# Optimization experiments

Hardware: AMD Instinct MI355X
Metric: run time of the kernel (lower is better)

Reference implementation:

```python
import jax, jax.numpy as jnp
import numpy as np

LN_EPS = 1e-5      # torch nn.LayerNorm default
NORM_EPS = 1e-12   # torch F.normalize default


def _layer_norm(x, gamma, beta):
    mu = jnp.mean(x, axis=-1, keepdims=True)
    var = jnp.mean((x - mu) ** 2, axis=-1, keepdims=True)
    return (x - mu) * jax.lax.rsqrt(var + LN_EPS) * gamma + beta


def _l2_normalize_rows(w):
    n = jnp.sqrt(jnp.sum(w * w, axis=1, keepdims=True))
    return w / jnp.maximum(n, NORM_EPS)


def setup_inputs() -> dict:
    key = jax.random.key(0)
    B, D = 32768, 512
    ks = jax.random.split(key, 4)
    return {
        "stimulus": jax.random.normal(ks[0], (B, D), dtype=jnp.float32),
        "prev_activation": jax.random.normal(ks[1], (B, D), dtype=jnp.float32),
        "W": jax.random.normal(ks[2], (D, D), dtype=jnp.float32),
        "Wr": jax.random.normal(ks[3], (D, D), dtype=jnp.float32),
        "alpha": jnp.full((D,), 0.1, dtype=jnp.float32),
        "decay": jnp.full((D,), 0.01, dtype=jnp.float32),
        "ln_act_gamma": jnp.ones((D,), dtype=jnp.float32),
        "ln_act_beta": jnp.zeros((D,), dtype=jnp.float32),
        "ln_rec_gamma": jnp.ones((D,), dtype=jnp.float32),
        "ln_rec_beta": jnp.zeros((D,), dtype=jnp.float32),
    }


def reference(stimulus, prev_activation, W, Wr, alpha, decay,
              ln_act_gamma, ln_act_beta, ln_rec_gamma, ln_rec_beta):
    # recurrent path
    rec_out = prev_activation @ Wr                      # [B, D]
    rec_norm = _layer_norm(rec_out, ln_rec_gamma, ln_rec_beta)
    # stimulus path
    stim_out = stimulus @ W                             # [B, D]
    final = jax.nn.relu(stim_out + rec_norm)
    final = _layer_norm(final, ln_act_gamma, ln_act_beta)

    # Hebbian weight update (detached in the original module)
    heb_upd = jnp.einsum('bi,bj->ij', stimulus, stim_out) * alpha[None, :]
    rec_upd = jnp.einsum('bi,bj->ij', prev_activation, rec_out) * alpha[None, :]
    # diag(decay) @ W is a row-wise broadcast scale
    new_W = _l2_normalize_rows(W + heb_upd - decay[:, None] * W)
    new_Wr = _l2_normalize_rows(Wr + rec_upd - decay[:, None] * Wr)

    return final, new_W, new_Wr
```

## Files before the change

### kernel.cpp

```cpp
#include <hip/hip_runtime.h>
#include <stdint.h>

typedef unsigned int u32;
typedef unsigned short u16;
typedef float  f32x4 __attribute__((ext_vector_type(4)));
typedef u32    u32x4 __attribute__((ext_vector_type(4)));
typedef __bf16 bf16x8 __attribute__((ext_vector_type(8)));

static __device__ __forceinline__ u16 f2bf(float f){
  u32 u = __builtin_bit_cast(u32, f);
  return (u16)((u + 0x7FFFu + ((u >> 16) & 1u)) >> 16);
}

static __device__ __forceinline__ void async16(const void* g, void* l){
  __builtin_amdgcn_global_load_lds((const __attribute__((address_space(1))) u32*)g,
                                   (__attribute__((address_space(3))) u32*)l, 16, 0, 0);
}

static __device__ __forceinline__ float wave_sum(float v){
#pragma unroll
  for (int o = 32; o > 0; o >>= 1) v += __shfl_xor(v, o, 64);
  return v;
}

__global__ __launch_bounds__(256) void k_cvt(const float* __restrict__ s0, const float* __restrict__ s1,
                                             u16* __restrict__ d0, u16* __restrict__ d1){
  const float* __restrict__ src = blockIdx.y ? s1 : s0;
  u16* __restrict__ dst = blockIdx.y ? d1 : d0;
  size_t i = ((size_t)blockIdx.x*256 + threadIdx.x) * 8;
  f32x4 a = *(const f32x4*)(src + i);
  f32x4 b = *(const f32x4*)(src + i + 4);
  u32x4 w;
  w[0] = (u32)f2bf(a[0]) | ((u32)f2bf(a[1]) << 16);
  w[1] = (u32)f2bf(a[2]) | ((u32)f2bf(a[3]) << 16);
  w[2] = (u32)f2bf(b[0]) | ((u32)f2bf(b[1]) << 16);
  w[3] = (u32)f2bf(b[2]) | ((u32)f2bf(b[3]) << 16);
  *(u32x4*)(dst + i) = w;
}

__global__ __launch_bounds__(256) void k_tp(const u16* __restrict__ s0, const u16* __restrict__ s1,
                                            u16* __restrict__ d0, u16* __restrict__ d1){
  const u16* __restrict__ src = blockIdx.z ? s1 : s0;
  u16* __restrict__ dst = blockIdx.z ? d1 : d0;
  __shared__ u32 st[64*128];
  const int r0 = blockIdx.x * 256;
  const int c0 = blockIdx.y * 64;
  const int t = threadIdx.x;
  const int tb = t & 127, th = t >> 7;
  const u16* pA = src + (size_t)(r0 + 2*tb)*512 + c0 + th*32;
  u32 a[16], b[16];
  {
    u32x4 a0 = *(const u32x4*)pA,        a1 = *(const u32x4*)(pA + 8);
    u32x4 a2 = *(const u32x4*)(pA + 16), a3 = *(const u32x4*)(pA + 24);
    u32x4 b0 = *(const u32x4*)(pA + 512),  b1 = *(const u32x4*)(pA + 520);
    u32x4 b2 = *(const u32x4*)(pA + 528),  b3 = *(const u32x4*)(pA + 536);
#pragma unroll
    for (int e = 0; e < 4; ++e){
      a[e] = a0[e]; a[4+e] = a1[e]; a[8+e] = a2[e]; a[12+e] = a3[e];
      b[e] = b0[e]; b[4+e] = b1[e]; b[8+e] = b2[e]; b[12+e] = b3[e];
    }
  }
  const int g5 = tb >> 2, w2 = tb & 3;
#pragma unroll
  for (int m = 0; m < 16; ++m){
    u32 lo = a[m], hi = b[m];
    u32 w0 = (lo & 0xFFFFu) | (hi << 16);
    u32 w1 = (lo >> 16) | (hi & 0xFFFF0000u);
    int d0i = th*32 + 2*m, d1i = d0i + 1;
    st[d0i*128 + ((g5 ^ (d0i & 7)) << 2) + w2] = w0;
    st[d1i*128 + ((g5 ^ (d1i & 7)) << 2) + w2] = w1;
  }
  __syncthreads();
  const int rd = t >> 2, rg = t & 3;
  u16* drow = dst + (size_t)(c0 + rd)*32768 + r0;
#pragma unroll
  for (int k = 0; k < 8; ++k){
    int gp = rg + 4*k;
    int slot = gp ^ (rd & 7);
    u32x4 w = *(const u32x4*)(st + rd*128 + slot*4);
    *(u32x4*)(drow + rg*8 + 32*k) = w;
  }
}

__global__ __launch_bounds__(256) void k_tcvt(const float* __restrict__ s0, const float* __restrict__ s1,
                                              u16* __restrict__ d0, u16* __restrict__ d1,
                                              int R, int C){
  const float* __restrict__ src = blockIdx.z ? s1 : s0;
  u16* __restrict__ dst = blockIdx.z ? d1 : d0;
  __shared__ u16 lt[64*72];
  const int c0 = blockIdx.x * 64, r0 = blockIdx.y * 64;
  const int tid = threadIdx.x;
  const int rr = tid >> 4, c4 = tid & 15;
#pragma unroll
  for (int p = 0; p < 4; ++p){
    int r = rr + p*16;
    f32x4 f = *(const f32x4*)(src + (size_t)(r0 + r)*C + c0 + c4*4);
#pragma unroll
    for (int e = 0; e < 4; ++e) lt[(c4*4 + e)*72 + r] = f2bf(f[e]);
  }
  __syncthreads();
  const int c = tid >> 2, bg = tid & 3;
  const u32x4* lp = (const u32x4*)(lt + c*72 + bg*16);
  u32x4 w0 = lp[0], w1 = lp[1];
  u16* drow = dst + (size_t)(c0 + c)*R + r0 + bg*16;
  *(u32x4*)drow = w0;
  *(u32x4*)(drow + 8) = w1;
}

__global__ __launch_bounds__(512) void k_gemm_fwd(const u16* __restrict__ SN, const u16* __restrict__ PN,
                                                  const u16* __restrict__ Wt, const u16* __restrict__ Wrt,
                                                  u16* __restrict__ SO, u16* __restrict__ RO,
                                                  u16* __restrict__ SOT, u16* __restrict__ ROT){
  __shared__ char smem[67584];
  u16* sA = (u16*)smem;
  u16* sB = (u16*)(smem + 32768);
  const int tid = threadIdx.x;
  const int lane = tid & 63, wid = tid >> 6;
  const int wm = wid >> 1, wn = wid & 1;
  const int l15 = lane & 15, q = lane >> 4;
  const int id = blockIdx.x;
  const int c8 = id & 7, g = id >> 3;
  const int sel = g >> 6, h = g & 63;
  const int yb = c8*16 + (h >> 2), xb = h & 3;
  const int m0 = yb * 256, n0 = xb * 128;
  const u16* __restrict__ A  = sel ? PN  : SN;
  const u16* __restrict__ Bt = sel ? Wrt : Wt;
  u16* __restrict__ Cn = sel ? RO  : SO;
  u16* __restrict__ Ct = sel ? ROT : SOT;

  f32x4 acc[4][4];
  const f32x4 vzero = {0.f, 0.f, 0.f, 0.f};
#pragma unroll
  for (int a = 0; a < 4; ++a)
#pragma unroll
    for (int b = 0; b < 4; ++b) acc[a][b] = vzero;

#pragma unroll 1
  for (int kt = 0; kt < 8; ++kt){
    const int k0 = kt*64;
#pragma unroll
    for (int it = 0; it < 4; ++it){
      int gg0 = it*512 + tid;
      int r = gg0 >> 3, gp = gg0 & 7, gsw = gp ^ (r & 7);
      async16(A + (size_t)(m0 + r)*512 + k0 + gsw*8, (char*)sA + (size_t)gg0*16);
    }
#pragma unroll
    for (int it = 0; it < 2; ++it){
      int gg0 = it*512 + tid;
      int r = gg0 >> 3, gp = gg0 & 7, gsw = gp ^ (r & 7);
      async16(Bt + (size_t)(n0 + r)*512 + k0 + gsw*8, (char*)sB + (size_t)gg0*16);
    }
    __syncthreads();
#pragma unroll
    for (int kk = 0; kk < 2; ++kk){
      bf16x8 af[4], bfv[4];
#pragma unroll
      for (int mt = 0; mt < 4; ++mt){
        int r = wm*64 + mt*16 + l15;
        int gsw = (kk*4 + q) ^ (r & 7);
        af[mt] = *(const bf16x8*)(sA + (size_t)(r*8 + gsw)*8);
      }
#pragma unroll
      for (int nt = 0; nt < 4; ++nt){
        int r = wn*64 + nt*16 + l15;
        int gsw = (kk*4 + q) ^ (r & 7);
        bfv[nt] = *(const bf16x8*)(sB + (size_t)(r*8 + gsw)*8);
      }
#pragma unroll
      for (int mt = 0; mt < 4; ++mt)
#pragma unroll
        for (int nt = 0; nt < 4; ++nt)
          acc[mt][nt] = __builtin_amdgcn_mfma_f32_16x16x32_bf16(af[mt], bfv[nt], acc[mt][nt], 0, 0, 0);
    }
    __syncthreads();
  }

  u16* lt = (u16*)smem;
#pragma unroll
  for (int mt = 0; mt < 4; ++mt)
#pragma unroll
    for (int nt = 0; nt < 4; ++nt){
      f32x4 v = acc[mt][nt];
      u16 b0 = f2bf(v[0]), b1 = f2bf(v[1]), b2 = f2bf(v[2]), b3 = f2bf(v[3]);
      int n = wn*64 + nt*16 + l15;
      int mb = wm*64 + mt*16 + q*4;
      u16* cn = Cn + (size_t)(m0 + mb)*512 + n0 + n;
      cn[0] = b0; cn[512] = b1; cn[1024] = b2; cn[1536] = b3;
      *(u32*)(lt + n*264 + mb)     = (u32)b0 | ((u32)b1 << 16);
      *(u32*)(lt + n*264 + mb + 2) = (u32)b2 | ((u32)b3 << 16);
    }
  __syncthreads();
#pragma unroll
  for (int p = 0; p < 8; ++p){
    int gg0 = p*512 + tid;
    int n = gg0 >> 5, mg = gg0 & 31;
    u32x4 w = *(const u32x4*)(lt + n*264 + mg*8);
    *(u32x4*)(Ct + (size_t)(n0 + n)*32768 + m0 + mg*8) = w;
  }
}

__global__ __launch_bounds__(512) void k_gemm_upd(const u16* __restrict__ A0, const u16* __restrict__ B0,
                                                  const u16* __restrict__ A1, const u16* __restrict__ B1,
                                                  float* __restrict__ part){
  __shared__ char smem[49152];
  u16* sA = (u16*)smem;
  u16* sB = (u16*)(smem + 16384);
  const int tid = threadIdx.x;
  const int lane = tid & 63, wid = tid >> 6;
  const int wm = wid >> 2, wn = wid & 3;
  const int l15 = lane & 15, q = lane >> 4;
  const int id = blockIdx.x;
  const int c8 = id & 7, g = id >> 3;
  const int zz = c8*8 + (g >> 3);
  const int xy = g & 7;
  const int mat = zz >> 5, sp = zz & 31;
  const int yb = xy & 3, xb = xy >> 2;
  const u16* __restrict__ A = mat ? A1 : A0;
  const u16* __restrict__ B = mat ? B1 : B0;
  const int m0 = yb * 128, n0 = xb * 256;
  const int kb = sp * 1024;

  f32x4 acc[4][4];
  const f32x4 vzero = {0.f, 0.f, 0.f, 0.f};
#pragma unroll
  for (int a = 0; a < 4; ++a)
#pragma unroll
    for (int b = 0; b < 4; ++b) acc[a][b] = vzero;

#pragma unroll 1
  for (int kt = 0; kt < 16; ++kt){
    const int k0 = kb + kt*64;
#pragma unroll
    for (int it = 0; it < 2; ++it){
      int gg0 = it*512 + tid;
      int r = gg0 >> 3, gp = gg0 & 7, gsw = gp ^ (r & 7);
      async16(A + (size_t)(m0 + r)*32768 + k0 + gsw*8, (char*)sA + (size_t)gg0*16);
    }
#pragma unroll
    for (int it = 0; it < 4; ++it){
      int gg0 = it*512 + tid;
      int r = gg0 >> 3, gp = gg0 & 7, gsw = gp ^ (r & 7);
      async16(B + (size_t)(n0 + r)*32768 + k0 + gsw*8, (char*)sB + (size_t)gg0*16);
    }
    __syncthreads();
#pragma unroll
    for (int kk = 0; kk < 2; ++kk){
      bf16x8 af[4], bfv[4];
#pragma unroll
      for (int mt = 0; mt < 4; ++mt){
        int r = wm*64 + mt*16 + l15;
        int gsw = (kk*4 + q) ^ (r & 7);
        af[mt] = *(const bf16x8*)(sA + (size_t)(r*8 + gsw)*8);
      }
#pragma unroll
      for (int nt = 0; nt < 4; ++nt){
        int r = wn*64 + nt*16 + l15;
        int gsw = (kk*4 + q) ^ (r & 7);
        bfv[nt] = *(const bf16x8*)(sB + (size_t)(r*8 + gsw)*8);
      }
#pragma unroll
      for (int mt = 0; mt < 4; ++mt)
#pragma unroll
        for (int nt = 0; nt < 4; ++nt)
          acc[mt][nt] = __builtin_amdgcn_mfma_f32_16x16x32_bf16(af[mt], bfv[nt], acc[mt][nt], 0, 0, 0);
    }
    __syncthreads();
  }

  float* dst = part + (size_t)(mat*32 + sp)*262144;
#pragma unroll
  for (int mt = 0; mt < 4; ++mt)
#pragma unroll
    for (int nt = 0; nt < 4; ++nt){
      f32x4 v = acc[mt][nt];
      int n = wn*64 + nt*16 + l15;
      int mb = wm*64 + mt*16 + q*4;
      float* d = dst + (size_t)(m0 + mb)*512 + n0 + n;
      d[0] = v[0]; d[512] = v[1]; d[1024] = v[2]; d[1536] = v[3];
    }
}

__global__ __launch_bounds__(256) void k_ln(const u16* __restrict__ SO, const u16* __restrict__ RO,
                                            const float* __restrict__ ga, const float* __restrict__ ba,
                                            const float* __restrict__ gr, const float* __restrict__ br,
                                            float* __restrict__ out){
  const int wid = threadIdx.x >> 6, lane = threadIdx.x & 63;
  const size_t b = (size_t)blockIdx.x*4 + wid;
  const int c = lane*8;
  float x[8], t[8];
  {
    u32x4 u = *(const u32x4*)(RO + b*512 + c);
#pragma unroll
    for (int i = 0; i < 4; ++i){
      u32 w = u[i];
      x[2*i]   = __uint_as_float(w << 16);
      x[2*i+1] = __uint_as_float(w & 0xFFFF0000u);
    }
  }
  float s = 0.f, ss = 0.f;
#pragma unroll
  for (int e = 0; e < 8; ++e){ s += x[e]; ss += x[e]*x[e]; }
  s = wave_sum(s); ss = wave_sum(ss);
  float mu = s*(1.f/512.f);
  float var = fmaxf(ss*(1.f/512.f) - mu*mu, 0.f);
  float rs = rsqrtf(var + 1e-5f);
  f32x4 g0 = *(const f32x4*)(gr + c), g1 = *(const f32x4*)(gr + c + 4);
  f32x4 h0 = *(const f32x4*)(br + c), h1 = *(const f32x4*)(br + c + 4);
  {
    u32x4 u = *(const u32x4*)(SO + b*512 + c);
    float so[8];
#pragma unroll
    for (int i = 0; i < 4; ++i){
      u32 w = u[i];
      so[2*i]   = __uint_as_float(w << 16);
      so[2*i+1] = __uint_as_float(w & 0xFFFF0000u);
    }
#pragma unroll
    for (int e = 0; e < 4; ++e) t[e]   = fmaxf(so[e]   + (x[e]  -mu)*rs*g0[e] + h0[e], 0.f);
#pragma unroll
    for (int e = 0; e < 4; ++e) t[4+e] = fmaxf(so[4+e] + (x[4+e]-mu)*rs*g1[e] + h1[e], 0.f);
  }
  float s2 = 0.f, ss2 = 0.f;
#pragma unroll
  for (int e = 0; e < 8; ++e){ s2 += t[e]; ss2 += t[e]*t[e]; }
  s2 = wave_sum(s2); ss2 = wave_sum(ss2);
  float mu2 = s2*(1.f/512.f);
  float var2 = fmaxf(ss2*(1.f/512.f) - mu2*mu2, 0.f);
  float rs2 = rsqrtf(var2 + 1e-5f);
  f32x4 G0 = *(const f32x4*)(ga + c), G1 = *(const f32x4*)(ga + c + 4);
  f32x4 H0 = *(const f32x4*)(ba + c), H1 = *(const f32x4*)(ba + c + 4);
  f32x4 o0, o1;
#pragma unroll
  for (int e = 0; e < 4; ++e){
    o0[e] = (t[e]   - mu2)*rs2*G0[e] + H0[e];
    o1[e] = (t[4+e] - mu2)*rs2*G1[e] + H1[e];
  }
  *(f32x4*)(out + b*512 + c)     = o0;
  *(f32x4*)(out + b*512 + c + 4) = o1;
}

__global__ __launch_bounds__(256) void k_finalize(const float* __restrict__ W0, const float* __restrict__ W1,
                                                  const float* __restrict__ part,
                                                  const float* __restrict__ alpha, const float* __restrict__ decay,
                                                  float* __restrict__ out){
  const int i = blockIdx.x, mat = blockIdx.y;
  const int t = threadIdx.x;
  const float* Wm = mat ? W1 : W0;
  const float* pb = part + (size_t)mat*32*262144 + (size_t)i*512;
  const float dc = decay[i];
  float v[2], ssq = 0.f;
#pragma unroll
  for (int h = 0; h < 2; ++h){
    int j = t + h*256;
    float acc = 0.f;
#pragma unroll
    for (int sp = 0; sp < 32; ++sp) acc += pb[(size_t)sp*262144 + j];
    float val = Wm[(size_t)i*512 + j]*(1.f - dc) + alpha[j]*acc;
    v[h] = val; ssq += val*val;
  }
  float wsum = wave_sum(ssq);
  __shared__ float red[4];
  const int lane = t & 63, wid = t >> 6;
  if (lane == 0) red[wid] = wsum;
  __syncthreads();
  float tot = red[0] + red[1] + red[2] + red[3];
  float rn = 1.f / fmaxf(sqrtf(tot), 1e-12f);
  out[(size_t)mat*262144 + (size_t)i*512 + t]       = v[0]*rn;
  out[(size_t)mat*262144 + (size_t)i*512 + t + 256] = v[1]*rn;
}

extern "C" void kernel_launch(void* const* d_in, const int* in_sizes, int n_in,
                              void* d_out, int out_size, void* d_ws, size_t ws_size,
                              hipStream_t stream) {
  const float* S  = (const float*)d_in[0];
  const float* P  = (const float*)d_in[1];
  const float* W  = (const float*)d_in[2];
  const float* Wr = (const float*)d_in[3];
  const float* alpha = (const float*)d_in[4];
  const float* decay = (const float*)d_in[5];
  const float* ga = (const float*)d_in[6];
  const float* ba = (const float*)d_in[7];
  const float* gr = (const float*)d_in[8];
  const float* br = (const float*)d_in[9];
  float* out = (float*)d_out;

  char* ws = (char*)d_ws;
  const size_t M32 = 33554432;
  const bool big = ws_size >= (size_t)269484032;

  u16 *SN, *PN, *ST, *PT, *SOT, *ROT, *SO, *RO, *Wt, *Wrt;
  if (big){
    SN  = (u16*)(ws);
    PN  = (u16*)(ws + 1*M32);
    ST  = (u16*)(ws + 2*M32);
    PT  = (u16*)(ws + 3*M32);
    SOT = (u16*)(ws + 4*M32);
    ROT = (u16*)(ws + 5*M32);
    SO  = (u16*)(ws + 6*M32);
    RO  = (u16*)(ws + 7*M32);
    Wt  = (u16*)(ws + 8*M32);
    Wrt = (u16*)(ws + 8*M32 + 524288);
  } else {
    SN  = (u16*)(ws);
    PN  = (u16*)(ws + 1*M32);
    SOT = (u16*)(ws + 2*M32);
    ROT = (u16*)(ws + 3*M32);
    SO  = (u16*)(ws + 4*M32);
    RO  = (u16*)(ws + 5*M32);
    Wt  = (u16*)(ws + 6*M32);
    Wrt = (u16*)(ws + 6*M32 + 524288);
    ST  = SO;
    PT  = RO;
  }
  float* part = (float*)ws;

  k_cvt<<<dim3(8192, 2), dim3(256), 0, stream>>>(S, P, SN, PN);
  if (big)
    k_tp<<<dim3(128, 8, 2), dim3(256), 0, stream>>>(SN, PN, ST, PT);
  k_tcvt<<<dim3(8, 8, 2), dim3(256), 0, stream>>>(W, Wr, Wt, Wrt, 512, 512);
  k_gemm_fwd<<<dim3(1024), dim3(512), 0, stream>>>(SN, PN, Wt, Wrt, SO, RO, SOT, ROT);
  k_ln<<<dim3(8192), dim3(256), 0, stream>>>(SO, RO, ga, ba, gr, br, out);
  if (!big)
    k_tp<<<dim3(128, 8, 2), dim3(256), 0, stream>>>(SN, PN, ST, PT);
  k_gemm_upd<<<dim3(512), dim3(512), 0, stream>>>(ST, SOT, PT, ROT, part);
  k_finalize<<<dim3(512, 2), dim3(256), 0, stream>>>(W, Wr, part, alpha, decay, out + 16777216);
}
```

Measured before the change: 346.1 us.

## Fuse input conversion, transpose and weight transpose into one prep kernel

Replaces the separate k_cvt, k_tp and k_tcvt launches with a single k_prep kernel whose blocks are split by index into row-major bf16 conversion, transposed conversion read straight from fp32, and weight transpose-conversion. The transposed copies are now built from the fp32 inputs rather than from the bf16 intermediate, which removes a dependency and two launches. In exchange the fp32 inputs are read twice, and the single shared-memory allocation may lower occupancy for the conversion blocks.

```diff
diff --git a/kernel.cpp b/kernel.cpp
--- a/kernel.cpp
+++ b/kernel.cpp
@@ -23,19 +23,123 @@
   return v;
 }
 
-__global__ __launch_bounds__(256) void k_cvt(const float* __restrict__ s0, const float* __restrict__ s1,
-                                             u16* __restrict__ d0, u16* __restrict__ d1){
-  const float* __restrict__ src = blockIdx.y ? s1 : s0;
-  u16* __restrict__ dst = blockIdx.y ? d1 : d0;
-  size_t i = ((size_t)blockIdx.x*256 + threadIdx.x) * 8;
-  f32x4 a = *(const f32x4*)(src + i);
-  f32x4 b = *(const f32x4*)(src + i + 4);
-  u32x4 w;
-  w[0] = (u32)f2bf(a[0]) | ((u32)f2bf(a[1]) << 16);
-  w[1] = (u32)f2bf(a[2]) | ((u32)f2bf(a[3]) << 16);
-  w[2] = (u32)f2bf(b[0]) | ((u32)f2bf(b[1]) << 16);
-  w[3] = (u32)f2bf(b[2]) | ((u32)f2bf(b[3]) << 16);
-  *(u32x4*)(dst + i) = w;
+
+static __device__ __forceinline__ void prep_cvt(int sub, const float* __restrict__ S,
+                                                const float* __restrict__ P,
+                                                u16* __restrict__ SN, u16* __restrict__ PN){
+  const size_t o0 = ((size_t)sub*256 + threadIdx.x) * 8;
+#pragma unroll
+  for (int j = 0; j < 4; ++j){
+    size_t o = o0 + (size_t)j*4194304;
+    f32x4 a = *(const f32x4*)(S + o);
+    f32x4 b = *(const f32x4*)(S + o + 4);
+    u32x4 w;
+    w[0] = (u32)f2bf(a[0]) | ((u32)f2bf(a[1]) << 16);
+    w[1] = (u32)f2bf(a[2]) | ((u32)f2bf(a[3]) << 16);
+    w[2] = (u32)f2bf(b[0]) | ((u32)f2bf(b[1]) << 16);
+    w[3] = (u32)f2bf(b[2]) | ((u32)f2bf(b[3]) << 16);
+    *(u32x4*)(SN + o) = w;
+  }
+#pragma unroll
+  for (int j = 0; j < 4; ++j){
+    size_t o = o0 + (size_t)j*4194304;
+    f32x4 a = *(const f32x4*)(P + o);
+    f32x4 b = *(const f32x4*)(P + o + 4);
+    u32x4 w;
+    w[0] = (u32)f2bf(a[0]) | ((u32)f2bf(a[1]) << 16);
+    w[1] = (u32)f2bf(a[2]) | ((u32)f2bf(a[3]) << 16);
+    w[2] = (u32)f2bf(b[0]) | ((u32)f2bf(b[1]) << 16);
+    w[3] = (u32)f2bf(b[2]) | ((u32)f2bf(b[3]) << 16);
+    *(u32x4*)(PN + o) = w;
+  }
+}
+
+static __device__ __forceinline__ void prep_tp(int sub, const float* __restrict__ S,
+                                               const float* __restrict__ P,
+                                               u16* __restrict__ ST, u16* __restrict__ PT,
+                                               u32* st){
+  const int bx = sub & 127, by = (sub >> 7) & 7, z = sub >> 10;
+  const float* __restrict__ src = z ? P : S;
+  u16* __restrict__ dst = z ? PT : ST;
+  const int r0 = bx * 256;
+  const int c0 = by * 64;
+  const int t = threadIdx.x;
+  const int tb = t & 127, th = t >> 7;
+  const float* pA = src + (size_t)(r0 + 2*tb)*512 + c0 + th*32;
+  float fa[32], fb[32];
+#pragma unroll
+  for (int c = 0; c < 8; ++c){
+    f32x4 va = *(const f32x4*)(pA + 4*c);
+    f32x4 vb = *(const f32x4*)(pA + 512 + 4*c);
+#pragma unroll
+    for (int e = 0; e < 4; ++e){ fa[4*c+e] = va[e]; fb[4*c+e] = vb[e]; }
+  }
+  const int g5 = tb >> 2, w2 = tb & 3;
+#pragma unroll
+  for (int m = 0; m < 16; ++m){
+    int d0i = th*32 + 2*m, d1i = d0i + 1;
+    u32 w0 = (u32)f2bf(fa[2*m])   | ((u32)f2bf(fb[2*m])   << 16);
+    u32 w1 = (u32)f2bf(fa[2*m+1]) | ((u32)f2bf(fb[2*m+1]) << 16);
+    st[d0i*128 + ((g5 ^ (d0i & 7)) << 2) + w2] = w0;
+    st[d1i*128 + ((g5 ^ (d1i & 7)) << 2) + w2] = w1;
+  }
+  __syncthreads();
+  const int rd = t >> 2, rg = t & 3;
+  u16* drow = dst + (size_t)(c0 + rd)*32768 + r0;
+#pragma unroll
+  for (int k = 0; k < 8; ++k){
+    int gp = rg + 4*k;
+    int slot = gp ^ (rd & 7);
+    u32x4 w = *(const u32x4*)(st + rd*128 + slot*4);
+    *(u32x4*)(drow + rg*8 + 32*k) = w;
+  }
+}
+
+static __device__ __forceinline__ void prep_tcvt(int sid, const float* __restrict__ W,
+                                                 const float* __restrict__ Wr,
+                                                 u16* __restrict__ Wt, u16* __restrict__ Wrt,
+                                                 u16* lt){
+  const int tix = sid & 7, tiy = (sid >> 3) & 7, tiz = sid >> 6;
+  const float* __restrict__ src = tiz ? Wr : W;
+  u16* __restrict__ dst = tiz ? Wrt : Wt;
+  const int c0 = tix * 64, r0 = tiy * 64;
+  const int tid = threadIdx.x;
+  const int rr = tid >> 4, c4 = tid & 15;
+#pragma unroll
+  for (int p = 0; p < 4; ++p){
+    int r = rr + p*16;
+    f32x4 f = *(const f32x4*)(src + (size_t)(r0 + r)*512 + c0 + c4*4);
+#pragma unroll
+    for (int e = 0; e < 4; ++e) lt[(c4*4 + e)*72 + r] = f2bf(f[e]);
+  }
+  __syncthreads();
+  const int c = tid >> 2, bg = tid & 3;
+  const u32x4* lp = (const u32x4*)(lt + c*72 + bg*16);
+  u32x4 w0 = lp[0], w1 = lp[1];
+  u16* drow = dst + (size_t)(c0 + c)*512 + r0 + bg*16;
+  *(u32x4*)drow = w0;
+  *(u32x4*)(drow + 8) = w1;
+}
+
+__global__ __launch_bounds__(256) void k_prep(const float* __restrict__ S, const float* __restrict__ P,
+                                              const float* __restrict__ W, const float* __restrict__ Wr,
+                                              u16* __restrict__ SN, u16* __restrict__ PN,
+                                              u16* __restrict__ ST, u16* __restrict__ PT,
+                                              u16* __restrict__ Wt, u16* __restrict__ Wrt,
+                                              int has_tp){
+  __shared__ char sm[32768];
+  const int id = blockIdx.x;
+  const int nmain = has_tp ? 4096 : 2048;
+  if (id < nmain){
+    if (has_tp){
+      if (id & 1) prep_cvt(id >> 1, S, P, SN, PN);
+      else        prep_tp(id >> 1, S, P, ST, PT, (u32*)sm);
+    } else {
+      prep_cvt(id, S, P, SN, PN);
+    }
+  } else {
+    prep_tcvt(id - nmain, W, Wr, Wt, Wrt, (u16*)sm);
+  }
 }
 
 __global__ __launch_bounds__(256) void k_tp(const u16* __restrict__ s0, const u16* __restrict__ s1,
@@ -80,31 +184,6 @@
     u32x4 w = *(const u32x4*)(st + rd*128 + slot*4);
     *(u32x4*)(drow + rg*8 + 32*k) = w;
   }
-}
-
-__global__ __launch_bounds__(256) void k_tcvt(const float* __restrict__ s0, const float* __restrict__ s1,
-                                              u16* __restrict__ d0, u16* __restrict__ d1,
-                                              int R, int C){
-  const float* __restrict__ src = blockIdx.z ? s1 : s0;
-  u16* __restrict__ dst = blockIdx.z ? d1 : d0;
-  __shared__ u16 lt[64*72];
-  const int c0 = blockIdx.x * 64, r0 = blockIdx.y * 64;
-  const int tid = threadIdx.x;
-  const int rr = tid >> 4, c4 = tid & 15;
-#pragma unroll
-  for (int p = 0; p < 4; ++p){
-    int r = rr + p*16;
-    f32x4 f = *(const f32x4*)(src + (size_t)(r0 + r)*C + c0 + c4*4);
-#pragma unroll
-    for (int e = 0; e < 4; ++e) lt[(c4*4 + e)*72 + r] = f2bf(f[e]);
-  }
-  __syncthreads();
-  const int c = tid >> 2, bg = tid & 3;
-  const u32x4* lp = (const u32x4*)(lt + c*72 + bg*16);
-  u32x4 w0 = lp[0], w1 = lp[1];
-  u16* drow = dst + (size_t)(c0 + c)*R + r0 + bg*16;
-  *(u32x4*)drow = w0;
-  *(u32x4*)(drow + 8) = w1;
 }
 
 __global__ __launch_bounds__(512) void k_gemm_fwd(const u16* __restrict__ SN, const u16* __restrict__ PN,
@@ -414,10 +493,7 @@
   }
   float* part = (float*)ws;
 
-  k_cvt<<<dim3(8192, 2), dim3(256), 0, stream>>>(S, P, SN, PN);
-  if (big)
-    k_tp<<<dim3(128, 8, 2), dim3(256), 0, stream>>>(SN, PN, ST, PT);
-  k_tcvt<<<dim3(8, 8, 2), dim3(256), 0, stream>>>(W, Wr, Wt, Wrt, 512, 512);
+  k_prep<<<dim3(big ? 4224 : 2176), dim3(256), 0, stream>>>(S, P, W, Wr, SN, PN, ST, PT, Wt, Wrt, big ? 1 : 0);
   k_gemm_fwd<<<dim3(1024), dim3(512), 0, stream>>>(SN, PN, Wt, Wrt, SO, RO, SOT, ROT);
   k_ln<<<dim3(8192), dim3(256), 0, stream>>>(SO, RO, ga, ba, gr, br, out);
   if (!big)
```

Result: slower. 378.5 us (+9.4%).
